# Performance work log

Hardware: AMD Instinct MI355X
Metric: run time of the kernel (lower is better)

## Reference

```python
import jax, jax.numpy as jnp
import numpy as np

B, C, N = 8, 256, 4096
DQK = C // 4  # 64
BN_EPS = 1e-5


def setup_inputs() -> dict:
    key = jax.random.key(0)
    ks = jax.random.split(key, 6)
    x = jax.random.normal(ks[0], (B, C, N), dtype=jnp.float32)
    # Conv1d kernel_size=1 weights, squeezed to [out, in]. q_conv and k_conv SHARE weights.
    Wqk = jax.random.normal(ks[1], (DQK, C), dtype=jnp.float32) * 0.05
    Wv = jax.random.normal(ks[2], (C, C), dtype=jnp.float32) * 0.05
    bv = jax.random.normal(ks[3], (C,), dtype=jnp.float32) * 0.01
    Wt = jax.random.normal(ks[4], (C, C), dtype=jnp.float32) * 0.05
    bt = jax.random.normal(ks[5], (C,), dtype=jnp.float32) * 0.01
    gamma = jnp.ones((C,), dtype=jnp.float32)
    beta = jnp.zeros((C,), dtype=jnp.float32)
    return {"x": x, "Wqk": Wqk, "Wv": Wv, "bv": bv, "Wt": Wt, "bt": bt,
            "gamma": gamma, "beta": beta}


def reference(x, Wqk, Wv, bv, Wt, bt, gamma, beta):
    # x: [B, C, N]
    x_q = jnp.einsum('bcn,dc->bnd', x, Wqk)              # [B, N, Dqk]
    x_k = jnp.einsum('bcn,dc->bdn', x, Wqk)              # [B, Dqk, N] (same weight)
    x_v = jnp.einsum('bcn,dc->bdn', x, Wv) + bv[None, :, None]  # [B, C, N]

    energy = jnp.einsum('bnd,bdm->bnm', x_q, x_k)        # [B, N, N]
    attention = jax.nn.softmax(energy, axis=-1)           # row softmax
    # L1 renorm over dim=1 (columns)
    attention = attention / (1e-9 + attention.sum(axis=1, keepdims=True))

    x_r = jnp.einsum('bcn,bnm->bcm', x_v, attention)      # [B, C, N]

    # trans_conv(x - x_r) -> BatchNorm1d (training-mode batch stats) -> ReLU
    t = jnp.einsum('bcn,dc->bdn', x - x_r, Wt) + bt[None, :, None]
    mean = t.mean(axis=(0, 2), keepdims=True)
    var = t.var(axis=(0, 2), keepdims=True)
    t = (t - mean) / jnp.sqrt(var + BN_EPS)
    t = t * gamma[None, :, None] + beta[None, :, None]
    x_r = jax.nn.relu(t)
    return x + x_r
```

## Files before the change

### kernel.cpp

```cpp
#include <hip/hip_runtime.h>
#include <hip/hip_bf16.h>

#define B_ 8
#define C_ 256
#define N_ 4096
#define D_ 64

typedef __attribute__((ext_vector_type(8))) short bf16x8;
typedef __attribute__((ext_vector_type(4))) float f32x4;

__device__ __forceinline__ float bf2f(unsigned short h){
    return __uint_as_float(((unsigned int)h) << 16);
}
__device__ __forceinline__ unsigned short f2bf(float f){
    unsigned int u = __float_as_uint(f);
    u += 0x7FFFu + ((u >> 16) & 1u);
    return (unsigned short)(u >> 16);
}
__device__ __forceinline__ bf16x8 ldf(const unsigned short* p){
    return *(const bf16x8*)p;
}
__device__ __forceinline__ f32x4 mfma_bf16(bf16x8 a, bf16x8 b, f32x4 c){
    return __builtin_amdgcn_mfma_f32_16x16x32_bf16(a, b, c, 0, 0, 0);
}
__device__ __forceinline__ void gld_lds16(const unsigned short* g, unsigned short* l){
    __builtin_amdgcn_global_load_lds(
        (const __attribute__((address_space(1))) unsigned int*)g,
        (__attribute__((address_space(3))) unsigned int*)l, 16, 0, 0);
}

__global__ __launch_bounds__(256) void convert_x_kernel(
    const float* __restrict__ x,
    unsigned short* __restrict__ xhT, unsigned short* __restrict__ xlT)
{
    __shared__ float tile[64][65];
    int b = blockIdx.z, c0 = blockIdx.y * 64, n0 = blockIdx.x * 64;
    int tid = threadIdx.x;
    int cc = tid & 63, rb = tid >> 6;
    #pragma unroll
    for (int j = 0; j < 16; j++){
        int rr = rb + 4*j;
        tile[rr][cc] = x[((size_t)(b*C_ + c0 + rr))*N_ + n0 + cc];
    }
    __syncthreads();
    #pragma unroll
    for (int j = 0; j < 16; j++){
        int rr = rb + 4*j;
        float v = tile[cc][rr];
        unsigned short h = f2bf(v);
        unsigned short l = f2bf(v - bf2f(h));
        size_t o = ((size_t)(b*N_ + n0 + rr))*C_ + c0 + cc;
        xhT[o] = h; xlT[o] = l;
    }
}

__global__ __launch_bounds__(256) void convert_w_kernel(
    const float* __restrict__ Wqk, const float* __restrict__ Wv, const float* __restrict__ Wt,
    unsigned short* __restrict__ Wqk_hi, unsigned short* __restrict__ Wqk_lo,
    unsigned short* __restrict__ Wv_b, unsigned short* __restrict__ Wt_b)
{
    int i = blockIdx.x * 256 + threadIdx.x;
    if (i < D_*C_){
        float v = Wqk[i];
        unsigned short h = f2bf(v);
        Wqk_hi[i] = h; Wqk_lo[i] = f2bf(v - bf2f(h));
    }
    int j = i - D_*C_;
    if (j >= 0 && j < C_*C_) Wv_b[j] = f2bf(Wv[j]);
    int k = j - C_*C_;
    if (k >= 0 && k < C_*C_) Wt_b[k] = f2bf(Wt[k]);
}

__global__ __launch_bounds__(256) void proj_qk_kernel(
    const unsigned short* __restrict__ xhT, const unsigned short* __restrict__ xlT,
    const unsigned short* __restrict__ Wh,  const unsigned short* __restrict__ Wl,
    unsigned short* __restrict__ qh, unsigned short* __restrict__ ql)
{
    int b = blockIdx.z, n0 = blockIdx.x * 64;
    int tid = threadIdx.x, w = tid >> 6, lane = tid & 63, q = lane >> 4, r = lane & 15;
    f32x4 z = {0.f,0.f,0.f,0.f};
    f32x4 acc[4] = {z,z,z,z};
    const unsigned short* Ah = Wh + (size_t)(16*w + r)*C_;
    const unsigned short* Al = Wl + (size_t)(16*w + r)*C_;
    const unsigned short* Bh = xhT + ((size_t)(b*N_ + n0 + r))*C_;
    const unsigned short* Bl = xlT + ((size_t)(b*N_ + n0 + r))*C_;
    for (int k0 = 0; k0 < C_; k0 += 32){
        bf16x8 ah = ldf(Ah + k0 + 8*q);
        bf16x8 al = ldf(Al + k0 + 8*q);
        #pragma unroll
        for (int f = 0; f < 4; f++){
            bf16x8 bh = ldf(Bh + (size_t)(16*f)*C_ + k0 + 8*q);
            bf16x8 bl = ldf(Bl + (size_t)(16*f)*C_ + k0 + 8*q);
            acc[f] = mfma_bf16(ah, bh, acc[f]);
            acc[f] = mfma_bf16(ah, bl, acc[f]);
            acc[f] = mfma_bf16(al, bh, acc[f]);
        }
    }
    #pragma unroll
    for (int f = 0; f < 4; f++){
        int col = n0 + 16*f + r;
        int d0 = 16*w + 4*q;
        size_t o = ((size_t)(b*N_ + col))*D_ + d0;
        ushort4 hv, lv;
        float v0 = acc[f][0], v1 = acc[f][1], v2 = acc[f][2], v3 = acc[f][3];
        hv.x = f2bf(v0); lv.x = f2bf(v0 - bf2f(hv.x));
        hv.y = f2bf(v1); lv.y = f2bf(v1 - bf2f(hv.y));
        hv.z = f2bf(v2); lv.z = f2bf(v2 - bf2f(hv.z));
        hv.w = f2bf(v3); lv.w = f2bf(v3 - bf2f(hv.w));
        *(ushort4*)(qh + o) = hv;
        *(ushort4*)(ql + o) = lv;
    }
}

__global__ __launch_bounds__(256) void qnorm_kernel(
    const unsigned short* __restrict__ qh, const unsigned short* __restrict__ ql,
    float* __restrict__ nrm)
{
    int rowg = blockIdx.x * 4 + (threadIdx.x >> 6);
    int lane = threadIdx.x & 63;
    float v = bf2f(qh[(size_t)rowg*D_ + lane]) + bf2f(ql[(size_t)rowg*D_ + lane]);
    float p = v*v;
    #pragma unroll
    for (int o = 1; o < 64; o <<= 1) p += __shfl_xor(p, o);
    if (lane == 0) nrm[rowg] = sqrtf(p);
}

__global__ __launch_bounds__(256) void qmax_kernel(
    const float* __restrict__ nrm, float* __restrict__ Mv)
{
    __shared__ float red[4];
    int b = blockIdx.x, tid = threadIdx.x, w = tid >> 6, lane = tid & 63;
    float m = 0.f;
    for (int i = tid; i < N_; i += 256) m = fmaxf(m, nrm[(size_t)b*N_ + i]);
    #pragma unroll
    for (int o = 1; o < 64; o <<= 1) m = fmaxf(m, __shfl_xor(m, o));
    if (lane == 0) red[w] = m;
    __syncthreads();
    if (tid == 0) Mv[b] = fmaxf(fmaxf(red[0], red[1]), fmaxf(red[2], red[3]));
}

__global__ __launch_bounds__(256) void proj_v_kernel(
    const unsigned short* __restrict__ xhT, const unsigned short* __restrict__ Wvb,
    const float* __restrict__ bv, unsigned short* __restrict__ xvb)
{
    int b = blockIdx.z, n0 = blockIdx.x * 64, d0 = blockIdx.y * 64;
    int tid = threadIdx.x, w = tid >> 6, lane = tid & 63, q = lane >> 4, r = lane & 15;
    f32x4 z = {0.f,0.f,0.f,0.f};
    f32x4 acc[4] = {z,z,z,z};
    const unsigned short* A = Wvb + (size_t)(d0 + 16*w + r)*C_;
    const unsigned short* Bb = xhT + ((size_t)(b*N_ + n0 + r))*C_;
    for (int k0 = 0; k0 < C_; k0 += 32){
        bf16x8 a = ldf(A + k0 + 8*q);
        #pragma unroll
        for (int f = 0; f < 4; f++){
            bf16x8 bb = ldf(Bb + (size_t)(16*f)*C_ + k0 + 8*q);
            acc[f] = mfma_bf16(a, bb, acc[f]);
        }
    }
    #pragma unroll
    for (int f = 0; f < 4; f++){
        int col = n0 + 16*f + r;
        #pragma unroll
        for (int i = 0; i < 4; i++){
            int row = d0 + 16*w + 4*q + i;
            float v = acc[f][i] + bv[row];
            xvb[((size_t)(b*C_ + row))*N_ + col] = f2bf(v);
        }
    }
}

__global__ __launch_bounds__(256) void rsum_kernel(
    const unsigned short* __restrict__ qh, const unsigned short* __restrict__ ql,
    const float* __restrict__ nrm, const float* __restrict__ Mv,
    float* __restrict__ rsum_part)
{
    __shared__ unsigned short Bh_lds[64*64];
    __shared__ unsigned short Bl_lds[64*64];
    int b = blockIdx.x, n0 = blockIdx.y * 128, ms = blockIdx.z;
    int tid = threadIdx.x, w = tid >> 6, lane = tid & 63, q = lane >> 4, r = lane & 15;
    int lrow = lane >> 3, lch = lane & 7;
    const unsigned short* qb = qh + (size_t)b*N_*D_;
    const unsigned short* lb = ql + (size_t)b*N_*D_;
    bf16x8 Ah[2][2], Al[2][2];
    #pragma unroll
    for (int g = 0; g < 2; g++){
        int row = n0 + 32*w + 16*g + r;
        const unsigned short* ap  = qb + (size_t)row*D_ + 8*q;
        const unsigned short* alp = lb + (size_t)row*D_ + 8*q;
        Ah[g][0] = ldf(ap);  Ah[g][1] = ldf(ap+32);
        Al[g][0] = ldf(alp); Al[g][1] = ldf(alp+32);
    }
    float M = Mv[b];
    float sh[2][4], rs[2][4];
    #pragma unroll
    for (int g = 0; g < 2; g++){
        float4 nv = *(const float4*)&nrm[(size_t)b*N_ + n0 + 32*w + 16*g + 4*q];
        sh[g][0] = nv.x*M; sh[g][1] = nv.y*M; sh[g][2] = nv.z*M; sh[g][3] = nv.w*M;
        rs[g][0] = rs[g][1] = rs[g][2] = rs[g][3] = 0.f;
    }
    f32x4 z = {0.f,0.f,0.f,0.f};
    for (int mt = 0; mt < 16; mt++){
        int m0 = ms*1024 + mt*64;
        #pragma unroll
        for (int i = 0; i < 2; i++){
            int row = i*32 + w*8 + lrow;
            int sc = lch ^ (row & 7);
            gld_lds16(qb + (size_t)(m0 + row)*D_ + sc*8, &Bh_lds[(i*32 + w*8)*64]);
            gld_lds16(lb + (size_t)(m0 + row)*D_ + sc*8, &Bl_lds[(i*32 + w*8)*64]);
        }
        __syncthreads();
        f32x4 e[2][4];
        #pragma unroll
        for (int g = 0; g < 2; g++)
            #pragma unroll
            for (int f = 0; f < 4; f++) e[g][f] = z;
        #pragma unroll
        for (int f = 0; f < 4; f++){
            int row = 16*f + r;
            int c0 = (q ^ (r & 7)) * 8;
            int c1 = ((4 + q) ^ (r & 7)) * 8;
            bf16x8 bh0 = *(bf16x8*)&Bh_lds[row*64 + c0];
            bf16x8 bh1 = *(bf16x8*)&Bh_lds[row*64 + c1];
            bf16x8 bl0 = *(bf16x8*)&Bl_lds[row*64 + c0];
            bf16x8 bl1 = *(bf16x8*)&Bl_lds[row*64 + c1];
            #pragma unroll
            for (int g = 0; g < 2; g++){
                e[g][f] = mfma_bf16(Ah[g][0], bh0, e[g][f]);
                e[g][f] = mfma_bf16(Ah[g][0], bl0, e[g][f]);
                e[g][f] = mfma_bf16(Al[g][0], bh0, e[g][f]);
                e[g][f] = mfma_bf16(Ah[g][1], bh1, e[g][f]);
                e[g][f] = mfma_bf16(Ah[g][1], bl1, e[g][f]);
                e[g][f] = mfma_bf16(Al[g][1], bh1, e[g][f]);
            }
        }
        #pragma unroll
        for (int g = 0; g < 2; g++)
            #pragma unroll
            for (int i = 0; i < 4; i++){
                rs[g][i] += __expf(e[g][0][i] - sh[g][i]) + __expf(e[g][1][i] - sh[g][i])
                          + __expf(e[g][2][i] - sh[g][i]) + __expf(e[g][3][i] - sh[g][i]);
            }
        __syncthreads();
    }
    #pragma unroll
    for (int g = 0; g < 2; g++)
        #pragma unroll
        for (int i = 0; i < 4; i++){
            #pragma unroll
            for (int o = 1; o < 16; o <<= 1) rs[g][i] += __shfl_xor(rs[g][i], o);
        }
    if (r == 0){
        #pragma unroll
        for (int g = 0; g < 2; g++){
            float4 v; v.x = rs[g][0]; v.y = rs[g][1]; v.z = rs[g][2]; v.w = rs[g][3];
            *(float4*)&rsum_part[((size_t)ms*B_ + b)*N_ + n0 + 32*w + 16*g + 4*q] = v;
        }
    }
}

__global__ __launch_bounds__(256) void shiftfin_kernel(
    const float* __restrict__ rsum_part, const float* __restrict__ nrm,
    const float* __restrict__ Mv, float* __restrict__ shift2)
{
    int gi = blockIdx.x * 256 + threadIdx.x;
    int b = gi >> 12;
    float s = rsum_part[gi] + rsum_part[(size_t)B_*N_ + gi]
            + rsum_part[(size_t)2*B_*N_ + gi] + rsum_part[(size_t)3*B_*N_ + gi];
    shift2[gi] = nrm[gi]*Mv[b] + __logf(s);
}

__global__ __launch_bounds__(256, 2) void pv_kernel(
    const unsigned short* __restrict__ qh, const unsigned short* __restrict__ ql,
    const unsigned short* __restrict__ xvb, const float* __restrict__ shift2,
    const float* __restrict__ x, unsigned short* __restrict__ uT)
{
    __shared__ unsigned short Pt[2][64*72];
    __shared__ float red[4][64];
    __shared__ float csinv[64];
    int b = blockIdx.x, m0 = blockIdx.y * 64;
    int tid = threadIdx.x, w = tid >> 6, lane = tid & 63, q = lane >> 4, r = lane & 15;
    const unsigned short* qb = qh + (size_t)b*N_*D_;
    const unsigned short* lb = ql + (size_t)b*N_*D_;
    bf16x8 Bh[4][2], Bl[4][2];
    #pragma unroll
    for (int f = 0; f < 4; f++){
        const unsigned short* bp  = qb + (size_t)(m0 + 16*f + r)*D_ + 8*q;
        const unsigned short* blp = lb + (size_t)(m0 + 16*f + r)*D_ + 8*q;
        Bh[f][0] = ldf(bp);  Bh[f][1] = ldf(bp+32);
        Bl[f][0] = ldf(blp); Bl[f][1] = ldf(blp+32);
    }
    const unsigned short* xvbase = xvb + (size_t)b*C_*N_;
    f32x4 z = {0.f,0.f,0.f,0.f};
    f32x4 accv[4][4];
    #pragma unroll
    for (int cf = 0; cf < 4; cf++)
        #pragma unroll
        for (int fm = 0; fm < 4; fm++) accv[cf][fm] = z;
    float cs[4] = {0.f,0.f,0.f,0.f};

    const unsigned short* ap0  = qb + (size_t)(16*w + r)*D_ + 8*q;
    const unsigned short* alp0 = lb + (size_t)(16*w + r)*D_ + 8*q;
    bf16x8 Ah0 = ldf(ap0), Ah1 = ldf(ap0+32), Al0 = ldf(alp0), Al1 = ldf(alp0+32);
    int buf = 0;

    for (int ns = 0; ns < N_; ns += 64){
        bf16x8 xvf[2][4];
        #pragma unroll
        for (int kc = 0; kc < 2; kc++)
            #pragma unroll
            for (int cf = 0; cf < 4; cf++)
                xvf[kc][cf] = ldf(xvbase + (size_t)(64*w + 16*cf + r)*N_ + ns + kc*32 + 8*q);
        f32x4 e[4] = {z,z,z,z};
        #pragma unroll
        for (int f = 0; f < 4; f++){
            e[f] = mfma_bf16(Ah0, Bh[f][0], e[f]);
            e[f] = mfma_bf16(Ah0, Bl[f][0], e[f]);
            e[f] = mfma_bf16(Al0, Bh[f][0], e[f]);
            e[f] = mfma_bf16(Ah1, Bh[f][1], e[f]);
            e[f] = mfma_bf16(Ah1, Bl[f][1], e[f]);
            e[f] = mfma_bf16(Al1, Bh[f][1], e[f]);
        }
        if (ns + 64 < N_){
            const unsigned short* ap  = qb + (size_t)(ns + 64 + 16*w + r)*D_ + 8*q;
            const unsigned short* alp = lb + (size_t)(ns + 64 + 16*w + r)*D_ + 8*q;
            Ah0 = ldf(ap); Ah1 = ldf(ap+32); Al0 = ldf(alp); Al1 = ldf(alp+32);
        }
        float4 s2 = *(const float4*)&shift2[(size_t)b*N_ + ns + 16*w + 4*q];
        float sh[4] = {s2.x, s2.y, s2.z, s2.w};
        #pragma unroll
        for (int f = 0; f < 4; f++){
            float p0 = __expf(e[f][0] - sh[0]);
            float p1 = __expf(e[f][1] - sh[1]);
            float p2 = __expf(e[f][2] - sh[2]);
            float p3 = __expf(e[f][3] - sh[3]);
            cs[f] += p0 + p1 + p2 + p3;
            ushort4 pv4;
            pv4.x = f2bf(p0); pv4.y = f2bf(p1); pv4.z = f2bf(p2); pv4.w = f2bf(p3);
            *(ushort4*)&Pt[buf][(16*f + r)*72 + 16*w + 4*q] = pv4;
        }
        __syncthreads();
        #pragma unroll
        for (int kc = 0; kc < 2; kc++){
            bf16x8 bfr[4];
            #pragma unroll
            for (int fm = 0; fm < 4; fm++)
                bfr[fm] = *(bf16x8*)&Pt[buf][(16*fm + r)*72 + kc*32 + 8*q];
            #pragma unroll
            for (int cf = 0; cf < 4; cf++)
                #pragma unroll
                for (int fm = 0; fm < 4; fm++)
                    accv[cf][fm] = mfma_bf16(xvf[kc][cf], bfr[fm], accv[cf][fm]);
        }
        buf ^= 1;
    }
    #pragma unroll
    for (int f = 0; f < 4; f++){
        float v = cs[f];
        v += __shfl_xor(v, 16);
        v += __shfl_xor(v, 32);
        if (q == 0) red[w][16*f + r] = v;
    }
    __syncthreads();
    if (tid < 64)
        csinv[tid] = 1.0f / (1e-9f + red[0][tid] + red[1][tid] + red[2][tid] + red[3][tid]);
    __syncthreads();
    #pragma unroll
    for (int fm = 0; fm < 4; fm++){
        int m = m0 + 16*fm + r;
        float inv = csinv[16*fm + r];
        #pragma unroll
        for (int cf = 0; cf < 4; cf++){
            int c0r = 64*w + 16*cf + 4*q;
            float u0 = x[(size_t)(b*C_ + c0r+0)*N_ + m] - accv[cf][fm][0]*inv;
            float u1 = x[(size_t)(b*C_ + c0r+1)*N_ + m] - accv[cf][fm][1]*inv;
            float u2 = x[(size_t)(b*C_ + c0r+2)*N_ + m] - accv[cf][fm][2]*inv;
            float u3 = x[(size_t)(b*C_ + c0r+3)*N_ + m] - accv[cf][fm][3]*inv;
            ushort4 uv;
            uv.x = f2bf(u0); uv.y = f2bf(u1); uv.z = f2bf(u2); uv.w = f2bf(u3);
            *(ushort4*)&uT[((size_t)b*N_ + m)*C_ + c0r] = uv;
        }
    }
}

__global__ __launch_bounds__(256) void t_stats_kernel(
    const unsigned short* __restrict__ uT, const unsigned short* __restrict__ Wtb,
    float* __restrict__ bnsum, float* __restrict__ bnsq)
{
    int b = blockIdx.z, n0 = blockIdx.x * 64, d0 = blockIdx.y * 64;
    int tid = threadIdx.x, w = tid >> 6, lane = tid & 63, q = lane >> 4, r = lane & 15;
    f32x4 z = {0.f,0.f,0.f,0.f};
    f32x4 acc[4] = {z,z,z,z};
    const unsigned short* A = Wtb + (size_t)(d0 + 16*w + r)*C_;
    const unsigned short* Bb = uT + ((size_t)(b*N_ + n0 + r))*C_;
    for (int k0 = 0; k0 < C_; k0 += 32){
        bf16x8 a = ldf(A + k0 + 8*q);
        #pragma unroll
        for (int f = 0; f < 4; f++){
            bf16x8 bb = ldf(Bb + (size_t)(16*f)*C_ + k0 + 8*q);
            acc[f] = mfma_bf16(a, bb, acc[f]);
        }
    }
    #pragma unroll
    for (int i = 0; i < 4; i++){
        float s = 0.f, s2 = 0.f;
        #pragma unroll
        for (int f = 0; f < 4; f++){ float v = acc[f][i]; s += v; s2 += v*v; }
        #pragma unroll
        for (int o = 1; o < 16; o <<= 1){ s += __shfl_xor(s, o); s2 += __shfl_xor(s2, o); }
        if (r == 0){
            int d = d0 + 16*w + 4*q + i;
            atomicAdd(&bnsum[d], s);
            atomicAdd(&bnsq[d], s2);
        }
    }
}

__global__ __launch_bounds__(256) void bn_final_kernel(
    const float* __restrict__ bnsum, const float* __restrict__ bnsq,
    const float* __restrict__ gamma, const float* __restrict__ beta,
    float* __restrict__ scale, float* __restrict__ shift)
{
    int d = threadIdx.x;
    const float inv = 1.0f / (B_ * N_);
    float m = bnsum[d] * inv;
    float v = bnsq[d] * inv - m*m;
    float rs = rsqrtf(v + 1e-5f);
    float sc = gamma[d] * rs;
    scale[d] = sc;
    shift[d] = beta[d] - m*sc;
}

__global__ __launch_bounds__(256) void final_kernel(
    const unsigned short* __restrict__ uT, const unsigned short* __restrict__ Wtb,
    const float* __restrict__ scale, const float* __restrict__ shift,
    const float* __restrict__ x, float* __restrict__ out)
{
    int b = blockIdx.z, n0 = blockIdx.x * 64, d0 = blockIdx.y * 64;
    int tid = threadIdx.x, w = tid >> 6, lane = tid & 63, q = lane >> 4, r = lane & 15;
    f32x4 z = {0.f,0.f,0.f,0.f};
    f32x4 acc[4] = {z,z,z,z};
    const unsigned short* A = Wtb + (size_t)(d0 + 16*w + r)*C_;
    const unsigned short* Bb = uT + ((size_t)(b*N_ + n0 + r))*C_;
    for (int k0 = 0; k0 < C_; k0 += 32){
        bf16x8 a = ldf(A + k0 + 8*q);
        #pragma unroll
        for (int f = 0; f < 4; f++){
            bf16x8 bb = ldf(Bb + (size_t)(16*f)*C_ + k0 + 8*q);
            acc[f] = mfma_bf16(a, bb, acc[f]);
        }
    }
    #pragma unroll
    for (int f = 0; f < 4; f++){
        int n = n0 + 16*f + r;
        #pragma unroll
        for (int i = 0; i < 4; i++){
            int d = d0 + 16*w + 4*q + i;
            float tv = acc[f][i]*scale[d] + shift[d];
            tv = fmaxf(tv, 0.0f);
            size_t o = ((size_t)(b*C_ + d))*N_ + n;
            out[o] = x[o] + tv;
        }
    }
}

extern "C" void kernel_launch(void* const* d_in, const int* in_sizes, int n_in,
                              void* d_out, int out_size, void* d_ws, size_t ws_size,
                              hipStream_t stream)
{
    const float* x     = (const float*)d_in[0];
    const float* Wqk   = (const float*)d_in[1];
    const float* Wv    = (const float*)d_in[2];
    const float* bv    = (const float*)d_in[3];
    const float* Wt    = (const float*)d_in[4];
    const float* gamma = (const float*)d_in[6];
    const float* beta  = (const float*)d_in[7];
    float* out = (float*)d_out;

    char* ws = (char*)d_ws;
    size_t off = 0;
    auto alloc = [&](size_t bytes) -> void* {
        void* p = ws + off;
        off += (bytes + 255) & ~(size_t)255;
        return p;
    };
    unsigned short* xhT    = (unsigned short*)alloc((size_t)B_*N_*C_*2);
    unsigned short* xlT    = (unsigned short*)alloc((size_t)B_*N_*C_*2);
    unsigned short* Wqk_hi = (unsigned short*)alloc((size_t)D_*C_*2);
    unsigned short* Wqk_lo = (unsigned short*)alloc((size_t)D_*C_*2);
    unsigned short* Wv_b   = (unsigned short*)alloc((size_t)C_*C_*2);
    unsigned short* Wt_b   = (unsigned short*)alloc((size_t)C_*C_*2);
    unsigned short* qh     = (unsigned short*)alloc((size_t)B_*N_*D_*2);
    unsigned short* ql     = (unsigned short*)alloc((size_t)B_*N_*D_*2);
    unsigned short* xvb    = (unsigned short*)alloc((size_t)B_*C_*N_*2);
    unsigned short* uT     = (unsigned short*)alloc((size_t)B_*N_*C_*2);
    float*          nrm    = (float*)alloc((size_t)B_*N_*4);
    float*          Mv     = (float*)alloc(B_*4);
    float*          rsum_part = (float*)alloc((size_t)4*B_*N_*4);
    float*          shift2 = (float*)alloc((size_t)B_*N_*4);
    float*          bnsum  = (float*)alloc(256*4);
    float*          bnsq   = (float*)alloc(256*4);
    float*          scale  = (float*)alloc(256*4);
    float*          shiftb = (float*)alloc(256*4);

    convert_x_kernel<<<dim3(N_/64, C_/64, B_), 256, 0, stream>>>(x, xhT, xlT);
    convert_w_kernel<<<(D_*C_ + 2*C_*C_ + 255)/256, 256, 0, stream>>>(
        Wqk, Wv, Wt, Wqk_hi, Wqk_lo, Wv_b, Wt_b);
    proj_qk_kernel<<<dim3(N_/64, 1, B_), 256, 0, stream>>>(xhT, xlT, Wqk_hi, Wqk_lo, qh, ql);
    qnorm_kernel<<<(B_*N_)/4, 256, 0, stream>>>(qh, ql, nrm);
    qmax_kernel<<<B_, 256, 0, stream>>>(nrm, Mv);
    proj_v_kernel<<<dim3(N_/64, C_/64, B_), 256, 0, stream>>>(xhT, Wv_b, bv, xvb);

    rsum_kernel<<<dim3(B_, N_/128, 4), 256, 0, stream>>>(qh, ql, nrm, Mv, rsum_part);
    shiftfin_kernel<<<(B_*N_)/256, 256, 0, stream>>>(rsum_part, nrm, Mv, shift2);
    pv_kernel<<<dim3(B_, N_/64), 256, 0, stream>>>(qh, ql, xvb, shift2, x, uT);

    hipMemsetAsync(bnsum, 0, 256*4, stream);
    hipMemsetAsync(bnsq, 0, 256*4, stream);
    t_stats_kernel<<<dim3(N_/64, C_/64, B_), 256, 0, stream>>>(uT, Wt_b, bnsum, bnsq);
    bn_final_kernel<<<1, 256, 0, stream>>>(bnsum, bnsq, gamma, beta, scale, shiftb);
    final_kernel<<<dim3(N_/64, C_/64, B_), 256, 0, stream>>>(uT, Wt_b, scale, shiftb, x, out);
}
```

Before: 509.4 us.

## Halve pv_kernel tile to 32 columns, raise occupancy, rotate key start

Each pv_kernel block now covers 32 output columns instead of 64. This doubles the grid to 1024 blocks, and the launch bound is raised to 4 blocks per SIMD so fewer registers and less shared memory are used per block. Each block also starts its key loop at a rotated offset to spread memory traffic across blocks, and it no longer prefetches the next Q fragment. The trade-off is that every block re-reads the full xv and Q streams for half the output work, which doubles global and L2 traffic for those operands. The bf16 packing also switches to the HIP intrinsic conversion.

After: 770.9 us. 51.3% more time.

```diff
diff --git a/kernel.cpp b/kernel.cpp
--- a/kernel.cpp
+++ b/kernel.cpp
@@ -269,21 +269,21 @@
     shift2[gi] = nrm[gi]*Mv[b] + __logf(s);
 }
 
-__global__ __launch_bounds__(256, 2) void pv_kernel(
+__global__ __launch_bounds__(256, 4) void pv_kernel(
     const unsigned short* __restrict__ qh, const unsigned short* __restrict__ ql,
     const unsigned short* __restrict__ xvb, const float* __restrict__ shift2,
     const float* __restrict__ x, unsigned short* __restrict__ uT)
 {
-    __shared__ unsigned short Pt[2][64*72];
-    __shared__ float red[4][64];
-    __shared__ float csinv[64];
-    int b = blockIdx.x, m0 = blockIdx.y * 64;
+    __shared__ unsigned short Pt[2][32*72];
+    __shared__ float red[4][32];
+    __shared__ float csinv[32];
+    int b = blockIdx.x, m0 = blockIdx.y * 32;
     int tid = threadIdx.x, w = tid >> 6, lane = tid & 63, q = lane >> 4, r = lane & 15;
     const unsigned short* qb = qh + (size_t)b*N_*D_;
     const unsigned short* lb = ql + (size_t)b*N_*D_;
-    bf16x8 Bh[4][2], Bl[4][2];
-    #pragma unroll
-    for (int f = 0; f < 4; f++){
+    bf16x8 Bh[2][2], Bl[2][2];
+    #pragma unroll
+    for (int f = 0; f < 2; f++){
         const unsigned short* bp  = qb + (size_t)(m0 + 16*f + r)*D_ + 8*q;
         const unsigned short* blp = lb + (size_t)(m0 + 16*f + r)*D_ + 8*q;
         Bh[f][0] = ldf(bp);  Bh[f][1] = ldf(bp+32);
@@ -291,28 +291,27 @@
     }
     const unsigned short* xvbase = xvb + (size_t)b*C_*N_;
     f32x4 z = {0.f,0.f,0.f,0.f};
-    f32x4 accv[4][4];
-    #pragma unroll
-    for (int cf = 0; cf < 4; cf++)
-        #pragma unroll
-        for (int fm = 0; fm < 4; fm++) accv[cf][fm] = z;
-    float cs[4] = {0.f,0.f,0.f,0.f};
-
-    const unsigned short* ap0  = qb + (size_t)(16*w + r)*D_ + 8*q;
-    const unsigned short* alp0 = lb + (size_t)(16*w + r)*D_ + 8*q;
-    bf16x8 Ah0 = ldf(ap0), Ah1 = ldf(ap0+32), Al0 = ldf(alp0), Al1 = ldf(alp0+32);
+    f32x4 accv[4][2];
+    #pragma unroll
+    for (int cf = 0; cf < 4; cf++){ accv[cf][0] = z; accv[cf][1] = z; }
+    float cs[2] = {0.f, 0.f};
+
+    int rot = (blockIdx.y & 63) * 64;
     int buf = 0;
-
-    for (int ns = 0; ns < N_; ns += 64){
+    for (int it = 0; it < 64; it++){
+        int ns = (it*64 + rot) & (N_ - 1);
+        const unsigned short* ap  = qb + (size_t)(ns + 16*w + r)*D_ + 8*q;
+        const unsigned short* alp = lb + (size_t)(ns + 16*w + r)*D_ + 8*q;
+        bf16x8 Ah0 = ldf(ap), Ah1 = ldf(ap+32), Al0 = ldf(alp), Al1 = ldf(alp+32);
         bf16x8 xvf[2][4];
         #pragma unroll
         for (int kc = 0; kc < 2; kc++)
             #pragma unroll
             for (int cf = 0; cf < 4; cf++)
                 xvf[kc][cf] = ldf(xvbase + (size_t)(64*w + 16*cf + r)*N_ + ns + kc*32 + 8*q);
-        f32x4 e[4] = {z,z,z,z};
-        #pragma unroll
-        for (int f = 0; f < 4; f++){
+        f32x4 e[2] = {z, z};
+        #pragma unroll
+        for (int f = 0; f < 2; f++){
             e[f] = mfma_bf16(Ah0, Bh[f][0], e[f]);
             e[f] = mfma_bf16(Ah0, Bl[f][0], e[f]);
             e[f] = mfma_bf16(Al0, Bh[f][0], e[f]);
@@ -320,52 +319,48 @@
             e[f] = mfma_bf16(Ah1, Bl[f][1], e[f]);
             e[f] = mfma_bf16(Al1, Bh[f][1], e[f]);
         }
-        if (ns + 64 < N_){
-            const unsigned short* ap  = qb + (size_t)(ns + 64 + 16*w + r)*D_ + 8*q;
-            const unsigned short* alp = lb + (size_t)(ns + 64 + 16*w + r)*D_ + 8*q;
-            Ah0 = ldf(ap); Ah1 = ldf(ap+32); Al0 = ldf(alp); Al1 = ldf(alp+32);
-        }
         float4 s2 = *(const float4*)&shift2[(size_t)b*N_ + ns + 16*w + 4*q];
         float sh[4] = {s2.x, s2.y, s2.z, s2.w};
         #pragma unroll
-        for (int f = 0; f < 4; f++){
+        for (int f = 0; f < 2; f++){
             float p0 = __expf(e[f][0] - sh[0]);
             float p1 = __expf(e[f][1] - sh[1]);
             float p2 = __expf(e[f][2] - sh[2]);
             float p3 = __expf(e[f][3] - sh[3]);
             cs[f] += p0 + p1 + p2 + p3;
-            ushort4 pv4;
-            pv4.x = f2bf(p0); pv4.y = f2bf(p1); pv4.z = f2bf(p2); pv4.w = f2bf(p3);
-            *(ushort4*)&Pt[buf][(16*f + r)*72 + 16*w + 4*q] = pv4;
+            union { __hip_bfloat162 h2[2]; ushort4 u4; } pk;
+            pk.h2[0] = __float22bfloat162_rn(make_float2(p0, p1));
+            pk.h2[1] = __float22bfloat162_rn(make_float2(p2, p3));
+            *(ushort4*)&Pt[buf][(16*f + r)*72 + 16*w + 4*q] = pk.u4;
         }
         __syncthreads();
         #pragma unroll
         for (int kc = 0; kc < 2; kc++){
-            bf16x8 bfr[4];
-            #pragma unroll
-            for (int fm = 0; fm < 4; fm++)
+            bf16x8 bfr[2];
+            #pragma unroll
+            for (int fm = 0; fm < 2; fm++)
                 bfr[fm] = *(bf16x8*)&Pt[buf][(16*fm + r)*72 + kc*32 + 8*q];
             #pragma unroll
             for (int cf = 0; cf < 4; cf++)
                 #pragma unroll
-                for (int fm = 0; fm < 4; fm++)
+                for (int fm = 0; fm < 2; fm++)
                     accv[cf][fm] = mfma_bf16(xvf[kc][cf], bfr[fm], accv[cf][fm]);
         }
         buf ^= 1;
     }
     #pragma unroll
-    for (int f = 0; f < 4; f++){
+    for (int f = 0; f < 2; f++){
         float v = cs[f];
         v += __shfl_xor(v, 16);
         v += __shfl_xor(v, 32);
         if (q == 0) red[w][16*f + r] = v;
     }
     __syncthreads();
-    if (tid < 64)
+    if (tid < 32)
         csinv[tid] = 1.0f / (1e-9f + red[0][tid] + red[1][tid] + red[2][tid] + red[3][tid]);
     __syncthreads();
     #pragma unroll
-    for (int fm = 0; fm < 4; fm++){
+    for (int fm = 0; fm < 2; fm++){
         int m = m0 + 16*fm + r;
         float inv = csinv[16*fm + r];
         #pragma unroll
@@ -512,7 +507,7 @@
 
     rsum_kernel<<<dim3(B_, N_/128, 4), 256, 0, stream>>>(qh, ql, nrm, Mv, rsum_part);
     shiftfin_kernel<<<(B_*N_)/256, 256, 0, stream>>>(rsum_part, nrm, Mv, shift2);
-    pv_kernel<<<dim3(B_, N_/64), 256, 0, stream>>>(qh, ql, xvb, shift2, x, uT);
+    pv_kernel<<<dim3(B_, N_/32), 256, 0, stream>>>(qh, ql, xvb, shift2, x, uT);
 
     hipMemsetAsync(bnsum, 0, 256*4, stream);
     hipMemsetAsync(bnsq, 0, 256*4, stream);
```
